# Performance work log

Hardware: AMD Instinct MI355X
Metric: run time of the kernel (lower is better)

Reference implementation:

```python
import jax, jax.numpy as jnp
import numpy as np

N = 10000      # atoms
E = 100000     # edges
C = 64         # hidden channels
S = 16         # spherical harmonic components (l_max=3)
NB = 8         # Bessel basis size
HID = 64       # radial MLP hidden
NE = 10        # chemical elements
G = 64         # graphs in batch
L = 2          # interaction layers
HEADS = 1
RC = 5.0       # radial cutoff
AVG_NEI = 16.0


def _sph_l3(u):
    # real spherical harmonics up to l=3, component normalization, on unit vectors u [E,3]
    x, y, z = u[..., 0], u[..., 1], u[..., 2]
    s3 = 3.0 ** 0.5; s5 = 5.0 ** 0.5; s15 = 15.0 ** 0.5
    c1 = (35.0 / 8.0) ** 0.5; c2 = 105.0 ** 0.5; c3 = (21.0 / 8.0) ** 0.5
    c4 = (7.0 / 4.0) ** 0.5; c5 = (105.0 / 4.0) ** 0.5
    comps = [jnp.ones_like(x),
             s3 * x, s3 * y, s3 * z,
             s15 * x * y, s15 * y * z, (s5 / 2) * (3 * z * z - 1), s15 * x * z, (s15 / 2) * (x * x - y * y),
             c1 * y * (3 * x * x - y * y), c2 * x * y * z, c3 * y * (5 * z * z - 1), c4 * z * (5 * z * z - 3),
             c3 * x * (5 * z * z - 1), c5 * z * (x * x - y * y), c1 * x * (x * x - 3 * y * y)]
    return jnp.stack(comps, axis=-1)  # [E, 16]


def _radial(r):
    # Bessel radial basis * polynomial cutoff (p=6); r [E,1] -> [E, NB]
    n = jnp.arange(1, NB + 1, dtype=r.dtype)
    bessel = (2.0 / RC) ** 0.5 * jnp.sin(n * jnp.pi * r / RC) / r
    t = r / RC
    p = 6.0
    fcut = 1.0 - (p + 1) * (p + 2) / 2 * t ** p + p * (p + 2) * t ** (p + 1) - p * (p + 1) / 2 * t ** (p + 2)
    fcut = jnp.where(r < RC, fcut, 0.0)
    return bessel * fcut


def setup_inputs() -> dict:
    key = jax.random.key(0)
    ks = jax.random.split(key, 20)
    positions = jax.random.uniform(ks[0], (N, 3), dtype=jnp.float32) * 6.0
    species = jax.random.randint(ks[1], (N,), 0, NE)
    node_attrs = jax.nn.one_hot(species, NE, dtype=jnp.float32)
    sender = jax.random.randint(ks[2], (E,), 0, N)
    offs = jax.random.randint(ks[3], (E,), 1, N)
    receiver = (sender + offs) % N  # no self loops
    edge_index = jnp.stack([sender, receiver]).astype(jnp.int32)
    batch = jnp.sort(jax.random.randint(ks[4], (N,), 0, G)).astype(jnp.int32)
    head = jnp.zeros((G,), jnp.int32)
    shifts = jnp.zeros((E, 3), jnp.float32)
    ptr = jnp.arange(G + 1, dtype=jnp.int32)
    w = 0.1
    return {
        'positions': positions, 'node_attrs': node_attrs, 'shifts': shifts,
        'atomic_energies': jax.random.normal(ks[5], (HEADS, NE), jnp.float32),
        'W_emb': w * jax.random.normal(ks[6], (NE, C), jnp.float32),
        'W_up': w * jax.random.normal(ks[7], (L, C, C), jnp.float32),
        'mlp_w1': w * jax.random.normal(ks[8], (L, NB, HID), jnp.float32),
        'mlp_w2': w * jax.random.normal(ks[9], (L, HID, HID), jnp.float32),
        'mlp_w3': w * jax.random.normal(ks[10], (L, HID, C * S), jnp.float32),
        'W_mix': w * jax.random.normal(ks[11], (L, C, C), jnp.float32),
        'W_skip': w * jax.random.normal(ks[12], (L, C, NE, C), jnp.float32),
        'Wc': w * jax.random.normal(ks[13], (L, NE, 3, C), jnp.float32),
        'W_out': w * jax.random.normal(ks[14], (L, C, C), jnp.float32),
        'W_ro': w * jax.random.normal(ks[15], (L, C, HEADS), jnp.float32),
        'edge_index': edge_index, 'batch': batch, 'head': head, 'ptr': ptr,
    }


def reference(positions, node_attrs, shifts, atomic_energies, W_emb, W_up, mlp_w1,
              mlp_w2, mlp_w3, W_mix, W_skip, Wc, W_out, W_ro,
              edge_index, batch, head, ptr):
    n_nodes = positions.shape[0]
    n_graphs = ptr.shape[0] - 1
    sender, receiver = edge_index[0], edge_index[1]
    na = jnp.arange(n_nodes)
    node_heads = head[batch]                                   # [N]
    # isolated-atom reference energies
    node_e0 = (node_attrs @ atomic_energies.T)[na, node_heads]  # [N]
    e0 = jax.ops.segment_sum(node_e0, batch, num_segments=n_graphs)
    node_feats = node_attrs @ W_emb                            # [N, C]
    # edge geometry: gather positions by edge index
    vectors = positions[receiver] - positions[sender] + shifts  # [E, 3]
    lengths = jnp.sqrt(jnp.sum(vectors ** 2, axis=-1, keepdims=True))  # [E, 1]
    edge_attrs = _sph_l3(vectors / lengths)                    # [E, S]
    edge_feats = _radial(lengths)                              # [E, NB]
    energies = [e0, jnp.zeros_like(e0)]  # e0, pair_energy (no pair_repulsion)
    for l in range(W_up.shape[0]):
        # radial MLP -> per-edge tensor-product weights
        h = jax.nn.silu(edge_feats @ mlp_w1[l])
        h = jax.nn.silu(h @ mlp_w2[l])
        tp_w = (h @ mlp_w3[l]).reshape(-1, C, S)               # [E, C, S]
        up = node_feats @ W_up[l]                              # [N, C]
        # gather-compute-scatter message passing
        msg = up[sender][:, :, None] * edge_attrs[:, None, :] * tp_w  # [E, C, S]
        A = jax.ops.segment_sum(msg, receiver, num_segments=n_nodes) / AVG_NEI
        A = jnp.einsum('ncs,cd->nds', A, W_mix[l])             # [N, C, S]
        # element-conditioned skip connection
        sc = jnp.einsum('nc,ced,ne->nd', node_feats, W_skip[l], node_attrs)
        # symmetric-contraction product basis (correlation up to 3), element-conditioned
        w = jnp.einsum('ne,ekc->nkc', node_attrs, Wc[l])       # [N, 3, C]
        p1 = A[:, :, 0]
        p2 = jnp.einsum('ncs,ncs->nc', A, A)
        p3 = p2 * p1
        node_feats = (w[:, 0] * p1 + w[:, 1] * p2 + w[:, 2] * p3) @ W_out[l] + sc
        node_en = (node_feats @ W_ro[l])[na, node_heads]       # [N]
        energies.append(jax.ops.segment_sum(node_en, batch, num_segments=n_graphs))
    contributions = jnp.stack(energies, axis=-1)               # [G, L+2]
    return jnp.sum(contributions, axis=-1)                     # [G]
```

## Files before the change

kernel.cpp:

```cpp
#include <hip/hip_runtime.h>

typedef unsigned short u16;
typedef unsigned int u32;
typedef __attribute__((ext_vector_type(8))) short short8;
typedef __attribute__((ext_vector_type(4))) float f32x4;

#define N_NODES 10000
#define N_EDGES 100000
#define C_CH 64
#define S_SPH 16
#define NB_R 8
#define HID_D 64
#define NE_EL 10
#define G_GR 64
#define L_LAY 2
#define N_HEADS 1
#define RCUT 5.0f
#define INV_AVG (1.0f/16.0f)

__device__ __forceinline__ u16 f2bf(float f) {
  u32 u = __float_as_uint(f);
  u32 r = (u + 0x7FFFu + ((u >> 16) & 1u)) >> 16;
  return (u16)r;
}

__global__ void k_init0(float* __restrict__ out, int* __restrict__ deg, int* __restrict__ bins) {
  int i = blockIdx.x * 256 + threadIdx.x;
  if (i < G_GR) out[i] = 0.0f;
  if (i < 64) bins[i] = 0;
  if (i < N_NODES) deg[i] = 0;
}

__global__ void k_node_init(const float* __restrict__ attrs, const float* __restrict__ ae,
                            const int* __restrict__ batch, const int* __restrict__ head,
                            int* __restrict__ species, float* __restrict__ out) {
  int n = blockIdx.x * 256 + threadIdx.x;
  if (n >= N_NODES) return;
  int sp = 0;
#pragma unroll
  for (int e = 0; e < NE_EL; ++e)
    if (attrs[n * NE_EL + e] > 0.5f) sp = e;
  species[n] = sp;
  int b = batch[n];
  int h = head[b];
  atomicAdd(&out[b], ae[h * NE_EL + sp]);
}

__global__ void k_embed(const int* __restrict__ species, const float* __restrict__ Wemb,
                        float* __restrict__ feats) {
  int idx = blockIdx.x * 256 + threadIdx.x;
  if (idx >= N_NODES * C_CH) return;
  feats[idx] = Wemb[species[idx >> 6] * C_CH + (idx & 63)];
}

__global__ void k_hist(const int* __restrict__ ei, int* __restrict__ deg) {
  int e = blockIdx.x * 256 + threadIdx.x;
  if (e >= N_EDGES) return;
  atomicAdd(&deg[ei[N_EDGES + e]], 1);
}

__global__ void __launch_bounds__(1024) k_scan(const int* __restrict__ deg,
                                               int* __restrict__ rowptr,
                                               int* __restrict__ woff) {
  __shared__ int wsum[16];
  __shared__ int carry_s;
  int tid = threadIdx.x;
  int lane = tid & 63, w = tid >> 6;
  if (tid == 0) carry_s = 0;
  __syncthreads();
  for (int base = 0; base < N_NODES; base += 1024) {
    int i = base + tid;
    int v = (i < N_NODES) ? deg[i] : 0;
    int orig = v;
#pragma unroll
    for (int off = 1; off < 64; off <<= 1) {
      int n = __shfl_up(v, off, 64);
      if (lane >= off) v += n;
    }
    if (lane == 63) wsum[w] = v;
    __syncthreads();
    if (w == 0 && lane < 16) {
      int x = wsum[lane];
#pragma unroll
      for (int off = 1; off < 16; off <<= 1) {
        int n = __shfl_up(x, off, 16);
        if (lane >= off) x += n;
      }
      wsum[lane] = x;
    }
    __syncthreads();
    int waveoff = (w > 0) ? wsum[w - 1] : 0;
    int carry = carry_s;
    int excl = carry + waveoff + v - orig;
    if (i < N_NODES) {
      rowptr[i] = excl;
      woff[i] = excl;
    }
    int tot = wsum[15];
    __syncthreads();
    if (tid == 0) carry_s = carry + tot;
    __syncthreads();
  }
  if (tid == 0) rowptr[N_NODES] = carry_s;
}

__global__ void k_degbin(const int* __restrict__ deg, int* __restrict__ bins) {
  int n = blockIdx.x * 256 + threadIdx.x;
  if (n >= N_NODES) return;
  int d = min(deg[n], 63);
  atomicAdd(&bins[63 - d], 1);
}

__global__ void __launch_bounds__(64) k_degscan(const int* __restrict__ bins,
                                                int* __restrict__ binoff) {
  int lane = threadIdx.x;
  int v = bins[lane];
  int orig = v;
#pragma unroll
  for (int off = 1; off < 64; off <<= 1) {
    int t = __shfl_up(v, off, 64);
    if (lane >= off) v += t;
  }
  binoff[lane] = v - orig;
}

__global__ void k_degscatter(const int* __restrict__ deg, int* __restrict__ binoff,
                             int* __restrict__ nodeOrder) {
  int n = blockIdx.x * 256 + threadIdx.x;
  if (n >= N_NODES) return;
  int d = min(deg[n], 63);
  int pos = atomicAdd(&binoff[63 - d], 1);
  nodeOrder[pos] = n;
}

__global__ void k_permute(const int* __restrict__ ei, int* __restrict__ woff,
                          int* __restrict__ rank, int* __restrict__ sndp) {
  int e = blockIdx.x * 256 + threadIdx.x;
  if (e >= N_EDGES) return;
  int rdst = ei[N_EDGES + e];
  int pos = atomicAdd(&woff[rdst], 1);
  rank[e] = pos;
  sndp[pos] = ei[e];
}

__global__ void k_geom(const float* __restrict__ pos, const float* __restrict__ shifts,
                       const int* __restrict__ ei, const int* __restrict__ rank,
                       float* __restrict__ Yp, float* __restrict__ radp) {
  int e = blockIdx.x * 256 + threadIdx.x;
  if (e >= N_EDGES) return;
  int s = ei[e], r = ei[N_EDGES + e];
  float dx = pos[r * 3 + 0] - pos[s * 3 + 0] + shifts[e * 3 + 0];
  float dy = pos[r * 3 + 1] - pos[s * 3 + 1] + shifts[e * 3 + 1];
  float dz = pos[r * 3 + 2] - pos[s * 3 + 2] + shifts[e * 3 + 2];
  float rr = sqrtf(dx * dx + dy * dy + dz * dz);
  rr = fmaxf(rr, 1e-12f);
  float inv = 1.0f / rr;
  float x = dx * inv, y = dy * inv, z = dz * inv;
  float xx = x * x, yy = y * y, zz = z * z;
  const float s3 = 1.73205080757f, s5 = 2.2360679775f, s15 = 3.87298334621f;
  const float c1 = 2.09165006634f, c2 = 10.2469507659f, c3 = 1.62018517461f;
  const float c4 = 1.32287565553f, c5 = 5.12347538298f;
  int rk = rank[e];
  float4* Yo = (float4*)(Yp + (size_t)rk * 16);
  Yo[0] = make_float4(1.0f, s3 * x, s3 * y, s3 * z);
  Yo[1] = make_float4(s15 * x * y, s15 * y * z, 0.5f * s5 * (3.0f * zz - 1.0f), s15 * x * z);
  Yo[2] = make_float4(0.5f * s15 * (xx - yy), c1 * y * (3.0f * xx - yy), c2 * x * y * z,
                      c3 * y * (5.0f * zz - 1.0f));
  Yo[3] = make_float4(c4 * z * (5.0f * zz - 3.0f), c3 * x * (5.0f * zz - 1.0f),
                      c5 * z * (xx - yy), c1 * x * (xx - 3.0f * yy));
  float t = rr * (1.0f / RCUT);
  float t2 = t * t;
  float t6 = t2 * t2 * t2;
  float fcut = 1.0f - 28.0f * t6 + 48.0f * t6 * t - 21.0f * t6 * t2;
  if (rr >= RCUT) fcut = 0.0f;
  float pref = 0.63245553203f * inv * fcut;
  float arg = 3.14159265359f * rr * (1.0f / RCUT);
  float sa, ca;
  __sincosf(arg, &sa, &ca);
  float twoc = 2.0f * ca;
  float sprev = 0.0f, scur = sa;
  float rv[8];
#pragma unroll
  for (int n = 0; n < 8; ++n) {
    rv[n] = pref * scur;
    float snext = twoc * scur - sprev;
    sprev = scur;
    scur = snext;
  }
  float4* Ro = (float4*)(radp + (size_t)rk * 8);
  Ro[0] = make_float4(rv[0], rv[1], rv[2], rv[3]);
  Ro[1] = make_float4(rv[4], rv[5], rv[6], rv[7]);
}

__global__ void k_prep(const float* __restrict__ w3, const float* __restrict__ w2,
                       const float* __restrict__ wmix, const float* __restrict__ wskip,
                       u16* __restrict__ w3t, u16* __restrict__ w2t, u16* __restrict__ wmixf,
                       float* __restrict__ wskt) {
  int idx = blockIdx.x * 256 + threadIdx.x;
  if (idx < L_LAY * 65536) {
    int l = idx >> 16;
    int r = idx & 65535;
    int k = r & 63;
    int c = (r >> 6) & 63;
    int s = r >> 12;
    w3t[idx] = f2bf(w3[(l * 64 + k) * 1024 + c * 16 + s]);
  } else if (idx < L_LAY * 65536 + L_LAY * 4096) {
    int i = idx - L_LAY * 65536;
    int l = i >> 12;
    int r = i & 4095;
    int t = r >> 6;
    int j = r & 63;
    w2t[l * 4096 + t * 64 + j] = f2bf(w2[(l * 64 + j) * 64 + t]);
  } else if (idx < L_LAY * 65536 + 2 * L_LAY * 4096) {
    int i = idx - L_LAY * 65536 - L_LAY * 4096;
    int l = i >> 12;
    int r = i & 4095;
    int j = r & 7;
    int col = (r >> 3) & 15;
    int kg = (r >> 7) & 3;
    int hf = (r >> 9) & 1;
    int dc = (r >> 10) & 3;
    int c = hf * 32 + kg * 8 + j;
    int d = dc * 16 + col;
    wmixf[l * 4096 + r] = f2bf(wmix[(l * 64 + c) * 64 + d]);
  } else if (idx < L_LAY * 65536 + 2 * L_LAY * 4096 + L_LAY * 40960) {
    int i = idx - (L_LAY * 65536 + 2 * L_LAY * 4096);
    int l = (i >= 40960) ? 1 : 0;
    int r = i - l * 40960;
    int e = r >> 12;
    int rem = r & 4095;
    int c = rem >> 6;
    int d = rem & 63;
    wskt[(size_t)l * 40960 + e * 4096 + c * 64 + d] =
        wskip[(size_t)l * 40960 + c * 640 + e * 64 + d];
  }
}

__global__ void __launch_bounds__(64) k_edge_mlp(const float* __restrict__ radp,
                                                 const float* __restrict__ w1,
                                                 const u16* __restrict__ w2T,
                                                 u16* __restrict__ h2) {
  __shared__ float w1s[NB_R * HID_D];
  __shared__ __align__(16) u16 h1b[16 * 64];
  int lane = threadIdx.x;
  for (int i = lane; i < NB_R * HID_D; i += 64) w1s[i] = w1[i];
  int er = lane & 15, jg = lane >> 4;
  int eb = blockIdx.x * 16;
  int e = eb + er;
  float4 ra = *(const float4*)(radp + (size_t)e * 8);
  float4 rb = *(const float4*)(radp + (size_t)e * 8 + 4);
  float rv[8] = {ra.x, ra.y, ra.z, ra.w, rb.x, rb.y, rb.z, rb.w};
  u32* hb = (u32*)h1b;
#pragma unroll
  for (int jj = 0; jj < 16; jj += 2) {
    float p0 = 0.f, p1 = 0.f;
#pragma unroll
    for (int k = 0; k < 8; ++k) {
      p0 += rv[k] * w1s[k * 64 + jg * 16 + jj];
      p1 += rv[k] * w1s[k * 64 + jg * 16 + jj + 1];
    }
    p0 = p0 / (1.f + __expf(-p0));
    p1 = p1 / (1.f + __expf(-p1));
    u32 packed = (u32)f2bf(p0) | ((u32)f2bf(p1) << 16);
    int d = jg * 8 + (jj >> 1);
    hb[er * 32 + (d ^ ((er & 7) << 2))] = packed;
  }
  int row = er, kg = jg, col = er;
  const u32* hbr = (const u32*)h1b;
  short8 a0 = *(const short8*)&hbr[row * 32 + ((kg * 4) ^ ((row & 7) << 2))];
  short8 a1 = *(const short8*)&hbr[row * 32 + ((16 + kg * 4) ^ ((row & 7) << 2))];
#pragma unroll
  for (int ch = 0; ch < 4; ++ch) {
    const u16* wp = w2T + (ch * 16 + col) * 64 + kg * 8;
    short8 b0 = *(const short8*)wp;
    short8 b1 = *(const short8*)(wp + 32);
    f32x4 acc = {0.f, 0.f, 0.f, 0.f};
    acc = __builtin_amdgcn_mfma_f32_16x16x32_bf16(a0, b0, acc, 0, 0, 0);
    acc = __builtin_amdgcn_mfma_f32_16x16x32_bf16(a1, b1, acc, 0, 0, 0);
#pragma unroll
    for (int rr = 0; rr < 4; ++rr) {
      float v = acc[rr];
      v = v / (1.f + __expf(-v));
      h2[(size_t)(eb + kg * 4 + rr) * 64 + ch * 16 + col] = f2bf(v);
    }
  }
}

__global__ void __launch_bounds__(256) k_up(const float* __restrict__ feats,
                                            const float* __restrict__ Wup,
                                            float* __restrict__ up) {
  __shared__ float ws[C_CH * C_CH];
  __shared__ float fs[4][C_CH];
  int tid = threadIdx.x;
  for (int i = tid; i < C_CH * C_CH; i += 256) ws[i] = Wup[i];
  __syncthreads();
  int slot = tid >> 6, t = tid & 63;
  for (int nb = blockIdx.x * 4; nb < N_NODES; nb += gridDim.x * 4) {
    int n = nb + slot;
    fs[slot][t] = feats[n * C_CH + t];
    float acc = 0.0f;
#pragma unroll
    for (int j = 0; j < C_CH; ++j) acc += fs[slot][j] * ws[j * C_CH + t];
    up[n * C_CH + t] = acc * INV_AVG;
  }
}

__global__ void __launch_bounds__(256) k_upe(const float* __restrict__ up,
                                             const int* __restrict__ sndp,
                                             float* __restrict__ upe) {
  int tid = threadIdx.x;
  int slot = tid >> 6, t = tid & 63;
  for (int pb = blockIdx.x * 4; pb < N_EDGES; pb += gridDim.x * 4) {
    int pos = pb + slot;
    upe[(size_t)pos * 64 + t] = up[(size_t)sndp[pos] * 64 + t];
  }
}

__global__ void __launch_bounds__(256) k_gather_fused(
    const u16* __restrict__ h2, const u16* __restrict__ W3T, const float* __restrict__ upe,
    const float* __restrict__ Yp, const int* __restrict__ rowptr,
    const int* __restrict__ nodeOrder, const u16* __restrict__ WmixF,
    const float* __restrict__ featsOld, float* __restrict__ featsNew,
    const float* __restrict__ WskT, const float* __restrict__ Wc,
    const float* __restrict__ WoutG, const float* __restrict__ Wro,
    const int* __restrict__ species, const int* __restrict__ batch,
    const int* __restrict__ headArr, float* __restrict__ out) {
  __shared__ __align__(16) u16 h2s[64 * 64];
  __shared__ __align__(16) float Yts[16][68];
  __shared__ __align__(16) u16 Asub[4][16][72];
  __shared__ float qs[4][64];
  __shared__ float fsub[4][64];
  __shared__ int rpsA[4], rpsB[4];
  int tid = threadIdx.x;
  int wv = tid >> 6, lane = tid & 63;
  int row = lane & 15, kg = lane >> 4;
  int col = row;
  int cg = wv;
  int cgc = cg * 16 + col;
  int nb = blockIdx.x * 4;
  int nodeW = nodeOrder[nb + wv];
  if (tid < 4) {
    int n = nodeOrder[nb + tid];
    rpsA[tid] = rowptr[n];
    rpsB[tid] = rowptr[n + 1];
  }
  fsub[wv][lane] = featsOld[(size_t)nodeW * 64 + lane];
  __syncthreads();
  int dmax = 0;
#pragma unroll
  for (int i = 0; i < 4; ++i) dmax = max(dmax, rpsB[i] - rpsA[i]);
  int rmax = max((dmax + 3) >> 2, 1);
  int baseR = rpsA[kg], degR = rpsB[kg] - rpsA[kg];

  float Areg[2][8];
#pragma unroll
  for (int hf = 0; hf < 2; ++hf)
#pragma unroll
    for (int ss = 0; ss < 8; ++ss) Areg[hf][ss] = 0.f;

  const u32* h2sr = (const u32*)h2s;

#pragma unroll 1
  for (int r0 = 0; r0 < rmax; r0 += 4) {
    int CH = min(4, rmax - r0);
    float uval[16];
#pragma unroll
    for (int rl = 0; rl < 4; ++rl)
#pragma unroll
      for (int q = 0; q < 4; ++q) {
        int slot = (r0 + rl) * 4 + q;
        int pos = min(baseR + slot, N_EDGES - 1);
        float u = upe[(size_t)pos * 64 + cgc];
        uval[rl * 4 + q] = (slot < degR) ? u : 0.f;
      }
    __syncthreads();
    for (int j = tid; j < 512; j += 256) {
      int rrow = j >> 3, part = j & 7;
      int node = rrow >> 4;
      int sl = r0 * 4 + (rrow & 15);
      int e = min(rpsA[node] + sl, N_EDGES - 1);
      short8 v = *(const short8*)(h2 + (size_t)e * 64 + part * 8);
      int dsw = (part * 4) ^ (((rrow ^ (rrow >> 3)) & 7) << 2);
      *(short8*)((u32*)h2s + rrow * 32 + dsw) = v;
    }
    {
      int rrow = tid >> 2, part = tid & 3;
      int node = rrow >> 4;
      int sl = r0 * 4 + (rrow & 15);
      int e = min(rpsA[node] + sl, N_EDGES - 1);
      float4 y = *(const float4*)(Yp + (size_t)e * 16 + part * 4);
      Yts[part * 4 + 0][rrow] = y.x;
      Yts[part * 4 + 1][rrow] = y.y;
      Yts[part * 4 + 2][rrow] = y.z;
      Yts[part * 4 + 3][rrow] = y.w;
    }
    __syncthreads();
#pragma unroll 1
    for (int hf = 0; hf < 2; ++hf) {
      short8 B0[8], B1[8];
#pragma unroll
      for (int ss = 0; ss < 8; ++ss) {
        int s = hf * 8 + ss;
        const u16* wp = W3T + (((s * 64 + cg * 16 + col) << 6) + kg * 8);
        B0[ss] = *(const short8*)wp;
        B1[ss] = *(const short8*)(wp + 32);
      }
#pragma unroll 1
      for (int rl = 0; rl < CH; ++rl) {
        int srow = (row >> 2) * 16 + rl * 4 + (row & 3);
        int swz = (((srow ^ (srow >> 3)) & 7) << 2);
        short8 a0 = *(const short8*)(h2sr + srow * 32 + ((kg * 4) ^ swz));
        short8 a1 = *(const short8*)(h2sr + srow * 32 + ((16 + kg * 4) ^ swz));
        float u0 = uval[rl * 4 + 0], u1 = uval[rl * 4 + 1];
        float u2 = uval[rl * 4 + 2], u3 = uval[rl * 4 + 3];
        int ybase = kg * 16 + rl * 4;
#pragma unroll
        for (int ss = 0; ss < 8; ++ss) {
          f32x4 acc = {0.f, 0.f, 0.f, 0.f};
          acc = __builtin_amdgcn_mfma_f32_16x16x32_bf16(a0, B0[ss], acc, 0, 0, 0);
          acc = __builtin_amdgcn_mfma_f32_16x16x32_bf16(a1, B1[ss], acc, 0, 0, 0);
          float4 yv = *(const float4*)&Yts[hf * 8 + ss][ybase];
          Areg[hf][ss] += acc[0] * yv.x * u0 + acc[1] * yv.y * u1 + acc[2] * yv.z * u2 +
                          acc[3] * yv.w * u3;
        }
      }
    }
  }
#pragma unroll
  for (int hf = 0; hf < 2; ++hf)
#pragma unroll
    for (int ss = 0; ss < 8; ++ss) Asub[kg][hf * 8 + ss][cg * 16 + col] = f2bf(Areg[hf][ss]);
  __syncthreads();

  int sp = species[nodeW];
  short8 a0m = *(const short8*)&Asub[wv][row][kg * 8];
  short8 a1m = *(const short8*)&Asub[wv][row][32 + kg * 8];
#pragma unroll
  for (int dc = 0; dc < 4; ++dc) {
    short8 wf0 = *(const short8*)(WmixF + (size_t)(dc * 1024 + 0 * 512 + kg * 128 + row * 8));
    short8 wf1 = *(const short8*)(WmixF + (size_t)(dc * 1024 + 1 * 512 + kg * 128 + row * 8));
    f32x4 acc = {0.f, 0.f, 0.f, 0.f};
    acc = __builtin_amdgcn_mfma_f32_16x16x32_bf16(a0m, wf0, acc, 0, 0, 0);
    acc = __builtin_amdgcn_mfma_f32_16x16x32_bf16(a1m, wf1, acc, 0, 0, 0);
    float psq = acc[0] * acc[0] + acc[1] * acc[1] + acc[2] * acc[2] + acc[3] * acc[3];
    psq += __shfl_xor(psq, 16, 64);
    psq += __shfl_xor(psq, 32, 64);
    float p1 = __shfl(acc[0], lane & 15, 64);
    float p3 = psq * p1;
    int d = dc * 16 + row;
    float qv = Wc[(sp * 3 + 0) * 64 + d] * p1 + Wc[(sp * 3 + 1) * 64 + d] * psq +
               Wc[(sp * 3 + 2) * 64 + d] * p3;
    if (kg == 0) qs[wv][d] = qv;
  }

  int t = lane;
  const float* wsk = WskT + (size_t)sp * 4096;
  float sc = 0.f;
#pragma unroll 8
  for (int c = 0; c < 64; ++c) sc += fsub[wv][c] * wsk[c * 64 + t];
  float v = sc;
#pragma unroll 8
  for (int d = 0; d < 64; ++d) v += qs[wv][d] * WoutG[d * 64 + t];
  featsNew[(size_t)nodeW * 64 + t] = v;
  int b = batch[nodeW];
  float en = v * Wro[t * N_HEADS + headArr[b]];
#pragma unroll
  for (int off = 32; off; off >>= 1) en += __shfl_down(en, off, 64);
  if (lane == 0) atomicAdd(&out[b], en);
}

extern "C" void kernel_launch(void* const* d_in, const int* in_sizes, int n_in,
                              void* d_out, int out_size, void* d_ws, size_t ws_size,
                              hipStream_t stream) {
  const float* pos = (const float*)d_in[0];
  const float* attrs = (const float*)d_in[1];
  const float* shifts = (const float*)d_in[2];
  const float* ae = (const float*)d_in[3];
  const float* Wemb = (const float*)d_in[4];
  const float* Wup = (const float*)d_in[5];
  const float* w1 = (const float*)d_in[6];
  const float* w2 = (const float*)d_in[7];
  const float* w3 = (const float*)d_in[8];
  const float* Wmix = (const float*)d_in[9];
  const float* Wskip = (const float*)d_in[10];
  const float* Wc = (const float*)d_in[11];
  const float* Wout = (const float*)d_in[12];
  const float* Wro = (const float*)d_in[13];
  const int* ei = (const int*)d_in[14];
  const int* batch = (const int*)d_in[15];
  const int* head = (const int*)d_in[16];
  float* out = (float*)d_out;

  char* p = (char*)d_ws;
  float* Yp = (float*)p;     p += (size_t)N_EDGES * 16 * 4;
  float* radp = (float*)p;   p += (size_t)N_EDGES * 8 * 4;
  float* up = (float*)p;     p += (size_t)N_NODES * 64 * 4;
  float* upe = (float*)p;    p += (size_t)N_EDGES * 64 * 4;
  float* fA = (float*)p;     p += (size_t)N_NODES * 64 * 4;
  float* fB = (float*)p;     p += (size_t)N_NODES * 64 * 4;
  u16* h2 = (u16*)p;         p += (size_t)N_EDGES * 64 * 2;
  u16* W3T = (u16*)p;        p += (size_t)L_LAY * 65536 * 2;
  u16* w2T = (u16*)p;        p += (size_t)L_LAY * 4096 * 2;
  u16* WmixF = (u16*)p;      p += (size_t)L_LAY * 4096 * 2;
  float* WskT = (float*)p;   p += (size_t)L_LAY * 40960 * 4;
  int* species = (int*)p;    p += (size_t)N_NODES * 4;
  int* deg = (int*)p;        p += (size_t)N_NODES * 4;
  int* rowptr = (int*)p;     p += (size_t)(N_NODES + 4) * 4;
  int* woff = (int*)p;       p += (size_t)N_NODES * 4;
  int* rank = (int*)p;       p += (size_t)N_EDGES * 4;
  int* sndp = (int*)p;       p += (size_t)N_EDGES * 4;
  int* bins = (int*)p;       p += 64 * 4;
  int* binoff = (int*)p;     p += 64 * 4;
  int* nodeOrder = (int*)p;  p += (size_t)N_NODES * 4;
  if ((size_t)(p - (char*)d_ws) > ws_size) return;

  k_init0<<<(N_NODES + 255) / 256, 256, 0, stream>>>(out, deg, bins);
  k_node_init<<<(N_NODES + 255) / 256, 256, 0, stream>>>(attrs, ae, batch, head, species, out);
  k_embed<<<(N_NODES * C_CH + 255) / 256, 256, 0, stream>>>(species, Wemb, fA);
  k_hist<<<(N_EDGES + 255) / 256, 256, 0, stream>>>(ei, deg);
  k_scan<<<1, 1024, 0, stream>>>(deg, rowptr, woff);
  k_degbin<<<(N_NODES + 255) / 256, 256, 0, stream>>>(deg, bins);
  k_degscan<<<1, 64, 0, stream>>>(bins, binoff);
  k_degscatter<<<(N_NODES + 255) / 256, 256, 0, stream>>>(deg, binoff, nodeOrder);
  k_permute<<<(N_EDGES + 255) / 256, 256, 0, stream>>>(ei, woff, rank, sndp);
  k_geom<<<(N_EDGES + 255) / 256, 256, 0, stream>>>(pos, shifts, ei, rank, Yp, radp);
  int prepTot = L_LAY * 65536 + 2 * L_LAY * 4096 + L_LAY * 40960;
  k_prep<<<(prepTot + 255) / 256, 256, 0, stream>>>(w3, w2, Wmix, Wskip, W3T, w2T, WmixF, WskT);

  const float* fOld = fA;
  float* fNew = fB;
  for (int l = 0; l < L_LAY; ++l) {
    k_edge_mlp<<<N_EDGES / 16, 64, 0, stream>>>(radp, w1 + l * NB_R * HID_D, w2T + l * 4096, h2);
    k_up<<<512, 256, 0, stream>>>(fOld, Wup + l * C_CH * C_CH, up);
    k_upe<<<2048, 256, 0, stream>>>(up, sndp, upe);
    k_gather_fused<<<N_NODES / 4, 256, 0, stream>>>(
        h2, W3T + l * 65536, upe, Yp, rowptr, nodeOrder, WmixF + l * 4096, fOld, fNew,
        WskT + (size_t)l * 40960, Wc + l * NE_EL * 3 * C_CH, Wout + l * C_CH * C_CH,
        Wro + l * C_CH * N_HEADS, species, batch, head, out);
    const float* tmp = fNew;
    fNew = (float*)fOld;
    fOld = tmp;
  }
}
```

Measured before the change: 459.1 us.

## Fuse edge MLP and up-projection gather into the per-node gather kernel

Removes the separate edge-MLP, node up-projection and per-edge gather kernels. The main gather kernel now computes the radial MLP per edge chunk with MFMA and the sender up-projection directly from bf16 node features with a pre-scaled bf16 Wup, writing both into shared memory. This drops the h2 and upe global round trips (about 38 MB of traffic per layer) and three launches. In exchange, the up-projection is recomputed per edge instead of per node, the node features and up values are held in bf16 (lower precision), and a block-wide sync is added per chunk.

After: 437.1 us (median of 3 runs). 1.05x faster.

```diff
diff --git a/kernel.cpp b/kernel.cpp
--- a/kernel.cpp
+++ b/kernel.cpp
@@ -24,6 +24,10 @@
   return (u16)r;
 }
 
+__device__ __forceinline__ float bf2f(u16 v) {
+  return __uint_as_float(((u32)v) << 16);
+}
+
 __global__ void k_init0(float* __restrict__ out, int* __restrict__ deg, int* __restrict__ bins) {
   int i = blockIdx.x * 256 + threadIdx.x;
   if (i < G_GR) out[i] = 0.0f;
@@ -47,10 +51,12 @@
 }
 
 __global__ void k_embed(const int* __restrict__ species, const float* __restrict__ Wemb,
-                        float* __restrict__ feats) {
+                        float* __restrict__ feats, u16* __restrict__ featsB) {
   int idx = blockIdx.x * 256 + threadIdx.x;
   if (idx >= N_NODES * C_CH) return;
-  feats[idx] = Wemb[species[idx >> 6] * C_CH + (idx & 63)];
+  float v = Wemb[species[idx >> 6] * C_CH + (idx & 63)];
+  feats[idx] = v;
+  featsB[idx] = f2bf(v);
 }
 
 __global__ void k_hist(const int* __restrict__ ei, int* __restrict__ deg) {
@@ -193,9 +199,10 @@
 }
 
 __global__ void k_prep(const float* __restrict__ w3, const float* __restrict__ w2,
-                       const float* __restrict__ wmix, const float* __restrict__ wskip,
-                       u16* __restrict__ w3t, u16* __restrict__ w2t, u16* __restrict__ wmixf,
-                       float* __restrict__ wskt) {
+                       const float* __restrict__ wmix, const float* __restrict__ wup,
+                       const float* __restrict__ wskip, u16* __restrict__ w3t,
+                       u16* __restrict__ w2t, u16* __restrict__ wmixf,
+                       u16* __restrict__ wupf, float* __restrict__ wskt) {
   int idx = blockIdx.x * 256 + threadIdx.x;
   if (idx < L_LAY * 65536) {
     int l = idx >> 16;
@@ -223,8 +230,20 @@
     int c = hf * 32 + kg * 8 + j;
     int d = dc * 16 + col;
     wmixf[l * 4096 + r] = f2bf(wmix[(l * 64 + c) * 64 + d]);
-  } else if (idx < L_LAY * 65536 + 2 * L_LAY * 4096 + L_LAY * 40960) {
-    int i = idx - (L_LAY * 65536 + 2 * L_LAY * 4096);
+  } else if (idx < L_LAY * 65536 + 3 * L_LAY * 4096) {
+    int i = idx - L_LAY * 65536 - 2 * L_LAY * 4096;
+    int l = i >> 12;
+    int r = i & 4095;
+    int j = r & 7;
+    int col = (r >> 3) & 15;
+    int kg = (r >> 7) & 3;
+    int hf = (r >> 9) & 1;
+    int dc = (r >> 10) & 3;
+    int c = hf * 32 + kg * 8 + j;
+    int d = dc * 16 + col;
+    wupf[l * 4096 + r] = f2bf(wup[(l * 64 + c) * 64 + d] * INV_AVG);
+  } else if (idx < L_LAY * 65536 + 3 * L_LAY * 4096 + L_LAY * 40960) {
+    int i = idx - (L_LAY * 65536 + 3 * L_LAY * 4096);
     int l = (i >= 40960) ? 1 : 0;
     int r = i - l * 40960;
     int e = r >> 12;
@@ -236,107 +255,32 @@
   }
 }
 
-__global__ void __launch_bounds__(64) k_edge_mlp(const float* __restrict__ radp,
-                                                 const float* __restrict__ w1,
-                                                 const u16* __restrict__ w2T,
-                                                 u16* __restrict__ h2) {
-  __shared__ float w1s[NB_R * HID_D];
-  __shared__ __align__(16) u16 h1b[16 * 64];
-  int lane = threadIdx.x;
-  for (int i = lane; i < NB_R * HID_D; i += 64) w1s[i] = w1[i];
-  int er = lane & 15, jg = lane >> 4;
-  int eb = blockIdx.x * 16;
-  int e = eb + er;
-  float4 ra = *(const float4*)(radp + (size_t)e * 8);
-  float4 rb = *(const float4*)(radp + (size_t)e * 8 + 4);
-  float rv[8] = {ra.x, ra.y, ra.z, ra.w, rb.x, rb.y, rb.z, rb.w};
-  u32* hb = (u32*)h1b;
-#pragma unroll
-  for (int jj = 0; jj < 16; jj += 2) {
-    float p0 = 0.f, p1 = 0.f;
-#pragma unroll
-    for (int k = 0; k < 8; ++k) {
-      p0 += rv[k] * w1s[k * 64 + jg * 16 + jj];
-      p1 += rv[k] * w1s[k * 64 + jg * 16 + jj + 1];
-    }
-    p0 = p0 / (1.f + __expf(-p0));
-    p1 = p1 / (1.f + __expf(-p1));
-    u32 packed = (u32)f2bf(p0) | ((u32)f2bf(p1) << 16);
-    int d = jg * 8 + (jj >> 1);
-    hb[er * 32 + (d ^ ((er & 7) << 2))] = packed;
-  }
-  int row = er, kg = jg, col = er;
-  const u32* hbr = (const u32*)h1b;
-  short8 a0 = *(const short8*)&hbr[row * 32 + ((kg * 4) ^ ((row & 7) << 2))];
-  short8 a1 = *(const short8*)&hbr[row * 32 + ((16 + kg * 4) ^ ((row & 7) << 2))];
-#pragma unroll
-  for (int ch = 0; ch < 4; ++ch) {
-    const u16* wp = w2T + (ch * 16 + col) * 64 + kg * 8;
-    short8 b0 = *(const short8*)wp;
-    short8 b1 = *(const short8*)(wp + 32);
-    f32x4 acc = {0.f, 0.f, 0.f, 0.f};
-    acc = __builtin_amdgcn_mfma_f32_16x16x32_bf16(a0, b0, acc, 0, 0, 0);
-    acc = __builtin_amdgcn_mfma_f32_16x16x32_bf16(a1, b1, acc, 0, 0, 0);
-#pragma unroll
-    for (int rr = 0; rr < 4; ++rr) {
-      float v = acc[rr];
-      v = v / (1.f + __expf(-v));
-      h2[(size_t)(eb + kg * 4 + rr) * 64 + ch * 16 + col] = f2bf(v);
-    }
-  }
-}
-
-__global__ void __launch_bounds__(256) k_up(const float* __restrict__ feats,
-                                            const float* __restrict__ Wup,
-                                            float* __restrict__ up) {
-  __shared__ float ws[C_CH * C_CH];
-  __shared__ float fs[4][C_CH];
-  int tid = threadIdx.x;
-  for (int i = tid; i < C_CH * C_CH; i += 256) ws[i] = Wup[i];
-  __syncthreads();
-  int slot = tid >> 6, t = tid & 63;
-  for (int nb = blockIdx.x * 4; nb < N_NODES; nb += gridDim.x * 4) {
-    int n = nb + slot;
-    fs[slot][t] = feats[n * C_CH + t];
-    float acc = 0.0f;
-#pragma unroll
-    for (int j = 0; j < C_CH; ++j) acc += fs[slot][j] * ws[j * C_CH + t];
-    up[n * C_CH + t] = acc * INV_AVG;
-  }
-}
-
-__global__ void __launch_bounds__(256) k_upe(const float* __restrict__ up,
-                                             const int* __restrict__ sndp,
-                                             float* __restrict__ upe) {
-  int tid = threadIdx.x;
-  int slot = tid >> 6, t = tid & 63;
-  for (int pb = blockIdx.x * 4; pb < N_EDGES; pb += gridDim.x * 4) {
-    int pos = pb + slot;
-    upe[(size_t)pos * 64 + t] = up[(size_t)sndp[pos] * 64 + t];
-  }
-}
-
-__global__ void __launch_bounds__(256) k_gather_fused(
-    const u16* __restrict__ h2, const u16* __restrict__ W3T, const float* __restrict__ upe,
-    const float* __restrict__ Yp, const int* __restrict__ rowptr,
-    const int* __restrict__ nodeOrder, const u16* __restrict__ WmixF,
-    const float* __restrict__ featsOld, float* __restrict__ featsNew,
+__global__ void __launch_bounds__(256) k_gather_mega(
+    const float* __restrict__ radp, const float* __restrict__ Yp,
+    const int* __restrict__ sndp, const u16* __restrict__ featsB,
+    const u16* __restrict__ W3T, const u16* __restrict__ w2T,
+    const u16* __restrict__ WupF, const float* __restrict__ w1,
+    const int* __restrict__ rowptr, const int* __restrict__ nodeOrder,
+    const u16* __restrict__ WmixF, const float* __restrict__ featsOld,
+    float* __restrict__ featsNew, u16* __restrict__ featsBN,
     const float* __restrict__ WskT, const float* __restrict__ Wc,
     const float* __restrict__ WoutG, const float* __restrict__ Wro,
     const int* __restrict__ species, const int* __restrict__ batch,
     const int* __restrict__ headArr, float* __restrict__ out) {
   __shared__ __align__(16) u16 h2s[64 * 64];
   __shared__ __align__(16) float Yts[16][68];
+  __shared__ __align__(16) u16 upL[64 * 72];
   __shared__ __align__(16) u16 Asub[4][16][72];
+  __shared__ float w1s[NB_R * HID_D];
   __shared__ float qs[4][64];
   __shared__ float fsub[4][64];
   __shared__ int rpsA[4], rpsB[4];
   int tid = threadIdx.x;
   int wv = tid >> 6, lane = tid & 63;
   int row = lane & 15, kg = lane >> 4;
+  int er = row, jg = kg;
   int col = row;
-  int cg = wv;
-  int cgc = cg * 16 + col;
+  int cgc = wv * 16 + col;
   int nb = blockIdx.x * 4;
   int nodeW = nodeOrder[nb + wv];
   if (tid < 4) {
@@ -344,56 +288,90 @@
     rpsA[tid] = rowptr[n];
     rpsB[tid] = rowptr[n + 1];
   }
+  for (int i = tid; i < NB_R * HID_D; i += 256) w1s[i] = w1[i];
   fsub[wv][lane] = featsOld[(size_t)nodeW * 64 + lane];
   __syncthreads();
   int dmax = 0;
 #pragma unroll
   for (int i = 0; i < 4; ++i) dmax = max(dmax, rpsB[i] - rpsA[i]);
   int rmax = max((dmax + 3) >> 2, 1);
-  int baseR = rpsA[kg], degR = rpsB[kg] - rpsA[kg];
+  int rpsAw = rpsA[wv];
+  int degW = rpsB[wv] - rpsAw;
+
+  u32* h1b = (u32*)&Asub[0][0][0] + wv * 512;
+  const u32* h2sr = (const u32*)h2s;
 
   float Areg[2][8];
 #pragma unroll
   for (int hf = 0; hf < 2; ++hf)
 #pragma unroll
     for (int ss = 0; ss < 8; ++ss) Areg[hf][ss] = 0.f;
-
-  const u32* h2sr = (const u32*)h2s;
 
 #pragma unroll 1
   for (int r0 = 0; r0 < rmax; r0 += 4) {
     int CH = min(4, rmax - r0);
-    float uval[16];
-#pragma unroll
-    for (int rl = 0; rl < 4; ++rl)
-#pragma unroll
-      for (int q = 0; q < 4; ++q) {
-        int slot = (r0 + rl) * 4 + q;
-        int pos = min(baseR + slot, N_EDGES - 1);
-        float u = upe[(size_t)pos * 64 + cgc];
-        uval[rl * 4 + q] = (slot < degR) ? u : 0.f;
+    int slotBase = r0 * 4;
+    __syncthreads();
+    int eW = min(rpsAw + slotBase + er, N_EDGES - 1);
+    float4 ra = *(const float4*)(radp + (size_t)eW * 8);
+    float4 rb = *(const float4*)(radp + (size_t)eW * 8 + 4);
+    float rv[8] = {ra.x, ra.y, ra.z, ra.w, rb.x, rb.y, rb.z, rb.w};
+#pragma unroll
+    for (int jj = 0; jj < 16; jj += 2) {
+      float p0 = 0.f, p1 = 0.f;
+#pragma unroll
+      for (int k = 0; k < 8; ++k) {
+        p0 += rv[k] * w1s[k * 64 + jg * 16 + jj];
+        p1 += rv[k] * w1s[k * 64 + jg * 16 + jj + 1];
       }
-    __syncthreads();
-    for (int j = tid; j < 512; j += 256) {
-      int rrow = j >> 3, part = j & 7;
-      int node = rrow >> 4;
-      int sl = r0 * 4 + (rrow & 15);
-      int e = min(rpsA[node] + sl, N_EDGES - 1);
-      short8 v = *(const short8*)(h2 + (size_t)e * 64 + part * 8);
-      int dsw = (part * 4) ^ (((rrow ^ (rrow >> 3)) & 7) << 2);
-      *(short8*)((u32*)h2s + rrow * 32 + dsw) = v;
-    }
-    {
-      int rrow = tid >> 2, part = tid & 3;
-      int node = rrow >> 4;
-      int sl = r0 * 4 + (rrow & 15);
-      int e = min(rpsA[node] + sl, N_EDGES - 1);
-      float4 y = *(const float4*)(Yp + (size_t)e * 16 + part * 4);
-      Yts[part * 4 + 0][rrow] = y.x;
-      Yts[part * 4 + 1][rrow] = y.y;
-      Yts[part * 4 + 2][rrow] = y.z;
-      Yts[part * 4 + 3][rrow] = y.w;
-    }
+      p0 = p0 / (1.f + __expf(-p0));
+      p1 = p1 / (1.f + __expf(-p1));
+      u32 packed = (u32)f2bf(p0) | ((u32)f2bf(p1) << 16);
+      int d = jg * 8 + (jj >> 1);
+      h1b[er * 32 + (d ^ ((er & 7) << 2))] = packed;
+    }
+    short8 ea0 = *(const short8*)&h1b[er * 32 + ((jg * 4) ^ ((er & 7) << 2))];
+    short8 ea1 = *(const short8*)&h1b[er * 32 + ((16 + jg * 4) ^ ((er & 7) << 2))];
+#pragma unroll
+    for (int ch = 0; ch < 4; ++ch) {
+      const u16* wp = w2T + (ch * 16 + er) * 64 + jg * 8;
+      short8 b0 = *(const short8*)wp;
+      short8 b1 = *(const short8*)(wp + 32);
+      f32x4 acc = {0.f, 0.f, 0.f, 0.f};
+      acc = __builtin_amdgcn_mfma_f32_16x16x32_bf16(ea0, b0, acc, 0, 0, 0);
+      acc = __builtin_amdgcn_mfma_f32_16x16x32_bf16(ea1, b1, acc, 0, 0, 0);
+#pragma unroll
+      for (int rr = 0; rr < 4; ++rr) {
+        float v = acc[rr];
+        v = v / (1.f + __expf(-v));
+        int R = wv * 16 + jg * 4 + rr;
+        int c = ch * 16 + er;
+        int g = (c >> 3) ^ ((R ^ (R >> 3)) & 7);
+        h2s[R * 64 + g * 8 + (er & 7)] = f2bf(v);
+      }
+    }
+    int snd = sndp[eW];
+    short8 fa0 = *(const short8*)(featsB + (size_t)snd * 64 + jg * 8);
+    short8 fa1 = *(const short8*)(featsB + (size_t)snd * 64 + 32 + jg * 8);
+#pragma unroll
+    for (int cgi = 0; cgi < 4; ++cgi) {
+      short8 wf0 = *(const short8*)(WupF + cgi * 1024 + jg * 128 + er * 8);
+      short8 wf1 = *(const short8*)(WupF + cgi * 1024 + 512 + jg * 128 + er * 8);
+      f32x4 acc = {0.f, 0.f, 0.f, 0.f};
+      acc = __builtin_amdgcn_mfma_f32_16x16x32_bf16(fa0, wf0, acc, 0, 0, 0);
+      acc = __builtin_amdgcn_mfma_f32_16x16x32_bf16(fa1, wf1, acc, 0, 0, 0);
+#pragma unroll
+      for (int r = 0; r < 4; ++r) {
+        int m = jg * 4 + r;
+        u16 uv = (slotBase + m < degW) ? f2bf(acc[r]) : (u16)0;
+        upL[(wv * 16 + m) * 72 + cgi * 16 + er] = uv;
+      }
+    }
+    float4 y = *(const float4*)(Yp + (size_t)eW * 16 + jg * 4);
+    Yts[jg * 4 + 0][wv * 16 + er] = y.x;
+    Yts[jg * 4 + 1][wv * 16 + er] = y.y;
+    Yts[jg * 4 + 2][wv * 16 + er] = y.z;
+    Yts[jg * 4 + 3][wv * 16 + er] = y.w;
     __syncthreads();
 #pragma unroll 1
     for (int hf = 0; hf < 2; ++hf) {
@@ -401,7 +379,7 @@
 #pragma unroll
       for (int ss = 0; ss < 8; ++ss) {
         int s = hf * 8 + ss;
-        const u16* wp = W3T + (((s * 64 + cg * 16 + col) << 6) + kg * 8);
+        const u16* wp = W3T + (((s * 64 + wv * 16 + col) << 6) + kg * 8);
         B0[ss] = *(const short8*)wp;
         B1[ss] = *(const short8*)(wp + 32);
       }
@@ -411,8 +389,10 @@
         int swz = (((srow ^ (srow >> 3)) & 7) << 2);
         short8 a0 = *(const short8*)(h2sr + srow * 32 + ((kg * 4) ^ swz));
         short8 a1 = *(const short8*)(h2sr + srow * 32 + ((16 + kg * 4) ^ swz));
-        float u0 = uval[rl * 4 + 0], u1 = uval[rl * 4 + 1];
-        float u2 = uval[rl * 4 + 2], u3 = uval[rl * 4 + 3];
+        float u0 = bf2f(upL[(kg * 16 + rl * 4 + 0) * 72 + cgc]);
+        float u1 = bf2f(upL[(kg * 16 + rl * 4 + 1) * 72 + cgc]);
+        float u2 = bf2f(upL[(kg * 16 + rl * 4 + 2) * 72 + cgc]);
+        float u3 = bf2f(upL[(kg * 16 + rl * 4 + 3) * 72 + cgc]);
         int ybase = kg * 16 + rl * 4;
 #pragma unroll
         for (int ss = 0; ss < 8; ++ss) {
@@ -429,7 +409,7 @@
 #pragma unroll
   for (int hf = 0; hf < 2; ++hf)
 #pragma unroll
-    for (int ss = 0; ss < 8; ++ss) Asub[kg][hf * 8 + ss][cg * 16 + col] = f2bf(Areg[hf][ss]);
+    for (int ss = 0; ss < 8; ++ss) Asub[kg][hf * 8 + ss][wv * 16 + col] = f2bf(Areg[hf][ss]);
   __syncthreads();
 
   int sp = species[nodeW];
@@ -462,6 +442,7 @@
 #pragma unroll 8
   for (int d = 0; d < 64; ++d) v += qs[wv][d] * WoutG[d * 64 + t];
   featsNew[(size_t)nodeW * 64 + t] = v;
+  featsBN[(size_t)nodeW * 64 + t] = f2bf(v);
   int b = batch[nodeW];
   float en = v * Wro[t * N_HEADS + headArr[b]];
 #pragma unroll
@@ -494,14 +475,14 @@
   char* p = (char*)d_ws;
   float* Yp = (float*)p;     p += (size_t)N_EDGES * 16 * 4;
   float* radp = (float*)p;   p += (size_t)N_EDGES * 8 * 4;
-  float* up = (float*)p;     p += (size_t)N_NODES * 64 * 4;
-  float* upe = (float*)p;    p += (size_t)N_EDGES * 64 * 4;
   float* fA = (float*)p;     p += (size_t)N_NODES * 64 * 4;
   float* fB = (float*)p;     p += (size_t)N_NODES * 64 * 4;
-  u16* h2 = (u16*)p;         p += (size_t)N_EDGES * 64 * 2;
+  u16* fBa = (u16*)p;        p += (size_t)N_NODES * 64 * 2;
+  u16* fBb = (u16*)p;        p += (size_t)N_NODES * 64 * 2;
   u16* W3T = (u16*)p;        p += (size_t)L_LAY * 65536 * 2;
   u16* w2T = (u16*)p;        p += (size_t)L_LAY * 4096 * 2;
   u16* WmixF = (u16*)p;      p += (size_t)L_LAY * 4096 * 2;
+  u16* WupF = (u16*)p;       p += (size_t)L_LAY * 4096 * 2;
   float* WskT = (float*)p;   p += (size_t)L_LAY * 40960 * 4;
   int* species = (int*)p;    p += (size_t)N_NODES * 4;
   int* deg = (int*)p;        p += (size_t)N_NODES * 4;
@@ -516,7 +497,7 @@
 
   k_init0<<<(N_NODES + 255) / 256, 256, 0, stream>>>(out, deg, bins);
   k_node_init<<<(N_NODES + 255) / 256, 256, 0, stream>>>(attrs, ae, batch, head, species, out);
-  k_embed<<<(N_NODES * C_CH + 255) / 256, 256, 0, stream>>>(species, Wemb, fA);
+  k_embed<<<(N_NODES * C_CH + 255) / 256, 256, 0, stream>>>(species, Wemb, fA, fBa);
   k_hist<<<(N_EDGES + 255) / 256, 256, 0, stream>>>(ei, deg);
   k_scan<<<1, 1024, 0, stream>>>(deg, rowptr, woff);
   k_degbin<<<(N_NODES + 255) / 256, 256, 0, stream>>>(deg, bins);
@@ -524,21 +505,21 @@
   k_degscatter<<<(N_NODES + 255) / 256, 256, 0, stream>>>(deg, binoff, nodeOrder);
   k_permute<<<(N_EDGES + 255) / 256, 256, 0, stream>>>(ei, woff, rank, sndp);
   k_geom<<<(N_EDGES + 255) / 256, 256, 0, stream>>>(pos, shifts, ei, rank, Yp, radp);
-  int prepTot = L_LAY * 65536 + 2 * L_LAY * 4096 + L_LAY * 40960;
-  k_prep<<<(prepTot + 255) / 256, 256, 0, stream>>>(w3, w2, Wmix, Wskip, W3T, w2T, WmixF, WskT);
+  int prepTot = L_LAY * 65536 + 3 * L_LAY * 4096 + L_LAY * 40960;
+  k_prep<<<(prepTot + 255) / 256, 256, 0, stream>>>(w3, w2, Wmix, Wup, Wskip, W3T, w2T, WmixF,
+                                                    WupF, WskT);
 
   const float* fOld = fA;
   float* fNew = fB;
+  const u16* fBOld = fBa;
+  u16* fBNew = fBb;
   for (int l = 0; l < L_LAY; ++l) {
-    k_edge_mlp<<<N_EDGES / 16, 64, 0, stream>>>(radp, w1 + l * NB_R * HID_D, w2T + l * 4096, h2);
-    k_up<<<512, 256, 0, stream>>>(fOld, Wup + l * C_CH * C_CH, up);
-    k_upe<<<2048, 256, 0, stream>>>(up, sndp, upe);
-    k_gather_fused<<<N_NODES / 4, 256, 0, stream>>>(
-        h2, W3T + l * 65536, upe, Yp, rowptr, nodeOrder, WmixF + l * 4096, fOld, fNew,
+    k_gather_mega<<<N_NODES / 4, 256, 0, stream>>>(
+        radp, Yp, sndp, fBOld, W3T + l * 65536, w2T + l * 4096, WupF + l * 4096,
+        w1 + l * NB_R * HID_D, rowptr, nodeOrder, WmixF + l * 4096, fOld, fNew, fBNew,
         WskT + (size_t)l * 40960, Wc + l * NE_EL * 3 * C_CH, Wout + l * C_CH * C_CH,
         Wro + l * C_CH * N_HEADS, species, batch, head, out);
-    const float* tmp = fNew;
-    fNew = (float*)fOld;
-    fOld = tmp;
-  }
-}
+    const float* tf = fNew; fNew = (float*)fOld; fOld = tf;
+    const u16* tb = fBNew; fBNew = (u16*)fBOld; fBOld = tb;
+  }
+}
```
